# Optimization experiments

Measured on AMD Instinct MI355X. Metric: run time of the kernel, lower is better.

## Reference

```python
import jax, jax.numpy as jnp
import numpy as np

COMMITMENT_COST = 0.25


def setup_inputs() -> dict:
    key = jax.random.key(0)
    k1, k2 = jax.random.split(key)
    B, D, H, W, K = 32, 64, 64, 64, 1024
    z_e = jax.random.normal(k1, (B, D, H, W), dtype=jnp.float32)
    # codebook initialized uniform(-1/K, 1/K) as in the torch module
    embedding = jax.random.uniform(k2, (K, D), dtype=jnp.float32,
                                   minval=-1.0 / K, maxval=1.0 / K)
    return {"z_e": z_e, "embedding": embedding}


def reference(z_e, embedding):
    B, D, H, W = z_e.shape
    # [B,D,H,W] -> [N, D] with N = B*H*W
    z_flat = jnp.transpose(z_e, (0, 2, 3, 1)).reshape(-1, D)
    # squared L2 distances [N, K] via expansion (same math as torch)
    dists = (jnp.sum(z_flat * z_flat, axis=1, keepdims=True)
             + jnp.sum(embedding * embedding, axis=1)
             - 2.0 * jnp.matmul(z_flat, embedding.T))
    indices_flat = jnp.argmin(dists, axis=1)            # [N]
    z_q_flat = embedding[indices_flat]                  # gather [N, D]
    z_q = jnp.transpose(z_q_flat.reshape(B, H, W, D), (0, 3, 1, 2))
    # straight-through estimator
    z_q_st = z_e + jax.lax.stop_gradient(z_q - z_e)
    vq_loss = jnp.mean((z_q - jax.lax.stop_gradient(z_e)) ** 2)
    commitment_loss = COMMITMENT_COST * jnp.mean((z_e - jax.lax.stop_gradient(z_q)) ** 2)
    indices = indices_flat.reshape(B, H, W)
    return z_q_st, indices, vq_loss, commitment_loss
```

## Files before the change

### kernel.cpp

```cpp
#include <hip/hip_runtime.h>

#define BB 32
#define DD 64
#define HWSZ 4096
#define KK 1024
#define NPIX (BB*HWSZ)
#define NELEM (NPIX*DD)

#define IDX_OUT_OFF NELEM
#define LOSS_OFF (IDX_OUT_OFF + NPIX)

#define WS_E2    0
#define WS_EBH   4096
#define WS_EBL   (WS_EBH + KK*DD*2)
#define WS_IDX   (WS_EBL + KK*DD*2)
#define WS_LIST  (WS_IDX + NPIX*4)
#define WS_CNT   (WS_LIST + NPIX*4)
#define WS_PART  (WS_CNT + 64)
#define WS_ZROWS (WS_PART + 8192)

#define PXB 128
#define ZSTR 129

#define BAND 2e-4f

typedef __attribute__((ext_vector_type(8))) short short8v;
typedef __attribute__((ext_vector_type(4))) float float4v;

__device__ __forceinline__ unsigned short bf16_rne(float f) {
    unsigned u = __float_as_uint(f);
    u += 0x7fffu + ((u >> 16) & 1u);
    return (unsigned short)(u >> 16);
}
__device__ __forceinline__ float bf16_tof(unsigned short h) {
    return __uint_as_float(((unsigned)h) << 16);
}

__device__ __forceinline__ float np_sumsq64(const float* a) {
#pragma clang fp contract(off)
    float r0=0.f,r1=0.f,r2=0.f,r3=0.f,r4=0.f,r5=0.f,r6=0.f,r7=0.f;
#pragma unroll
    for (int i = 0; i < 64; i += 8) {
        r0 += a[i+0]*a[i+0]; r1 += a[i+1]*a[i+1];
        r2 += a[i+2]*a[i+2]; r3 += a[i+3]*a[i+3];
        r4 += a[i+4]*a[i+4]; r5 += a[i+5]*a[i+5];
        r6 += a[i+6]*a[i+6]; r7 += a[i+7]*a[i+7];
    }
    return ((r0+r1)+(r2+r3))+((r4+r5)+(r6+r7));
}

__device__ __forceinline__ float np_sumsq64_lds(const float* sh) {
#pragma clang fp contract(off)
    float r0=0.f,r1=0.f,r2=0.f,r3=0.f,r4=0.f,r5=0.f,r6=0.f,r7=0.f;
#pragma unroll
    for (int i = 0; i < 64; i += 8) {
        float a0=sh[i+0],a1=sh[i+1],a2=sh[i+2],a3=sh[i+3];
        float a4=sh[i+4],a5=sh[i+5],a6=sh[i+6],a7=sh[i+7];
        r0 += a0*a0; r1 += a1*a1; r2 += a2*a2; r3 += a3*a3;
        r4 += a4*a4; r5 += a5*a5; r6 += a6*a6; r7 += a7*a7;
    }
    return ((r0+r1)+(r2+r3))+((r4+r5)+(r6+r7));
}

__device__ __forceinline__ float np_sumsq64_str(const float* sh, int stride) {
#pragma clang fp contract(off)
    float r0=0.f,r1=0.f,r2=0.f,r3=0.f,r4=0.f,r5=0.f,r6=0.f,r7=0.f;
#pragma unroll
    for (int i = 0; i < 64; i += 8) {
        float a0=sh[(i+0)*stride],a1=sh[(i+1)*stride];
        float a2=sh[(i+2)*stride],a3=sh[(i+3)*stride];
        float a4=sh[(i+4)*stride],a5=sh[(i+5)*stride];
        float a6=sh[(i+6)*stride],a7=sh[(i+7)*stride];
        r0 += a0*a0; r1 += a1*a1; r2 += a2*a2; r3 += a3*a3;
        r4 += a4*a4; r5 += a5*a5; r6 += a6*a6; r7 += a7*a7;
    }
    return ((r0+r1)+(r2+r3))+((r4+r5)+(r6+r7));
}

__global__ __launch_bounds__(256) void vq_e2(const float* __restrict__ emb,
                                             float* __restrict__ e2) {
    int k = blockIdx.x * blockDim.x + threadIdx.x;
    float ek[DD];
    const float4* p = reinterpret_cast<const float4*>(emb + (size_t)k * DD);
#pragma unroll
    for (int q = 0; q < 16; ++q) {
        float4 v = p[q];
        ek[4*q+0]=v.x; ek[4*q+1]=v.y; ek[4*q+2]=v.z; ek[4*q+3]=v.w;
    }
    e2[k] = np_sumsq64(ek);
}

__global__ __launch_bounds__(256) void vq_bfrag(const float* __restrict__ emb,
                                                short* __restrict__ ebh,
                                                short* __restrict__ ebl) {
    int t    = blockIdx.x * 256 + threadIdx.x;
    int l    = t & 63;
    int slot = t >> 6;
    int ct = slot >> 1, ks = slot & 1;
    int code  = ct*16 + (l & 15);
    int dbase = ks*32 + (l >> 4)*8;
    const float* ep = emb + (size_t)code*DD + dbase;
    short8v h, lo;
#pragma unroll
    for (int j = 0; j < 8; ++j) {
        float v = ep[j];
        unsigned short hh = bf16_rne(v);
        h[j]  = (short)hh;
        lo[j] = (short)bf16_rne(v - bf16_tof(hh));
    }
    ((short8v*)ebh)[t] = h;
    ((short8v*)ebl)[t] = lo;
}

__global__ __launch_bounds__(256) void vq_main(
        const float* __restrict__ z, const float* __restrict__ emb,
        const short* __restrict__ ebh, const short* __restrict__ ebl,
        const float* __restrict__ e2,
        int* __restrict__ idx, int* __restrict__ list, int* __restrict__ cnt,
        float* __restrict__ zrows, int zcap,
        float* __restrict__ out, double* __restrict__ partial) {
    __shared__ float zsh[DD * ZSTR];
    __shared__ int   idx_loc[PXB];
    __shared__ int   flpx[128], flslot[128];
    __shared__ int   q_px[128], q_k1[128], q_k2[128];
    __shared__ int   nfl, n2c;
    __shared__ double sred[256];
    const int tid = threadIdx.x;
    const int w   = tid >> 6;
    const int l   = tid & 63;
    const int lr  = l & 15;
    const int lg  = l >> 4;
    const int b   = blockIdx.x >> 5;
    const int hw0 = (blockIdx.x & 31) * PXB;
    const float* zb = z + (size_t)b*(DD*HWSZ) + hw0;

    if (tid == 0) { nfl = 0; n2c = 0; }
    {
        const int row = tid >> 7, col = tid & 127;
#pragma unroll 8
        for (int d0 = 0; d0 < DD; d0 += 2)
            zsh[(d0+row)*ZSTR + col] = zb[(size_t)(d0+row)*HWSZ + col];
    }
    __syncthreads();

    short8v ah[2][2], al[2][2];
#pragma unroll
    for (int rt = 0; rt < 2; ++rt) {
#pragma unroll
        for (int ks = 0; ks < 2; ++ks) {
            int px = w*32 + rt*16 + lr;
            int dbase = ks*32 + lg*8;
#pragma unroll
            for (int j = 0; j < 8; ++j) {
                float v = zsh[(dbase + j)*ZSTR + px];
                unsigned short hh = bf16_rne(v);
                ah[rt][ks][j] = (short)hh;
                al[rt][ks][j] = (short)bf16_rne(v - bf16_tof(hh));
            }
        }
    }

    float b1a[2][4], b2a[2][4], b3a[2][4];
#pragma unroll
    for (int rt = 0; rt < 2; ++rt)
#pragma unroll
        for (int r = 0; r < 4; ++r) {
            b1a[rt][r] = 3.4e38f; b2a[rt][r] = 3.4e38f; b3a[rt][r] = 3.4e38f;
        }

    const short8v* EBH = (const short8v*)ebh;
    const short8v* EBL = (const short8v*)ebl;

    short8v bh0 = EBH[l],  bh1 = EBH[64 + l];
    short8v bl0 = EBL[l],  bl1 = EBL[64 + l];
    float   e2c = e2[lr];

#pragma unroll 1
    for (int ct = 0; ct < 64; ++ct) {
        int ctn = (ct + 1) & 63;
        int s0  = ctn*128 + l;
        short8v nh0 = EBH[s0], nh1 = EBH[s0+64];
        short8v nl0 = EBL[s0], nl1 = EBL[s0+64];
        float   ne2 = e2[ctn*16 + lr];

        const unsigned kf = (unsigned)(ct*16 + lr);
        const unsigned kr = kf ^ 1023u;
#pragma unroll
        for (int rt = 0; rt < 2; ++rt) {
            float4v acc = {0.f, 0.f, 0.f, 0.f};
            acc = __builtin_amdgcn_mfma_f32_16x16x32_bf16(ah[rt][0], bh0, acc, 0,0,0);
            acc = __builtin_amdgcn_mfma_f32_16x16x32_bf16(ah[rt][1], bh1, acc, 0,0,0);
            acc = __builtin_amdgcn_mfma_f32_16x16x32_bf16(ah[rt][0], bl0, acc, 0,0,0);
            acc = __builtin_amdgcn_mfma_f32_16x16x32_bf16(ah[rt][1], bl1, acc, 0,0,0);
            acc = __builtin_amdgcn_mfma_f32_16x16x32_bf16(al[rt][0], bh0, acc, 0,0,0);
            acc = __builtin_amdgcn_mfma_f32_16x16x32_bf16(al[rt][1], bh1, acc, 0,0,0);
#pragma unroll
            for (int r = 0; r < 4; ++r) {
                float s = __builtin_fmaf(-2.f, acc[r], e2c);
                unsigned su = __float_as_uint(s) & ~1023u;
                unsigned kk = ((int)su < 0) ? kr : kf;
                float p = __uint_as_float(su | kk);
                float ob2 = b2a[rt][r];
                b3a[rt][r] = fminf(b3a[rt][r], fmaxf(ob2, p));
                b2a[rt][r] = fmaxf(b1a[rt][r], fminf(ob2, p));
                b1a[rt][r] = fminf(b1a[rt][r], p);
            }
        }
        bh0 = nh0; bh1 = nh1; bl0 = nl0; bl1 = nl1; e2c = ne2;
    }

#pragma unroll
    for (int rt = 0; rt < 2; ++rt) {
#pragma unroll
        for (int r = 0; r < 4; ++r) {
            float b1 = b1a[rt][r], b2 = b2a[rt][r], b3 = b3a[rt][r];
#pragma unroll
            for (int m = 1; m < 16; m <<= 1) {
                float o1 = __shfl_xor(b1, m, 64);
                float o2 = __shfl_xor(b2, m, 64);
                float o3 = __shfl_xor(b3, m, 64);
                float mx  = fmaxf(b1, o1);
                float mn2 = fminf(b2, o2);
                float n1 = fminf(b1, o1);
                float n2 = fminf(mx, mn2);
                float n3 = fminf(fminf(fmaxf(mn2, mx), fmaxf(b2, o2)),
                                 fminf(b3, o3));
                b1 = n1; b2 = n2; b3 = n3;
            }
            if (lr == 0) {
                unsigned u1 = __float_as_uint(b1);
                int i1 = (int)(u1 & 1023u); if ((int)u1 < 0) i1 ^= 1023;
                int pxl = w*32 + rt*16 + lg*4 + r;
                int n   = b*HWSZ + hw0 + pxl;
                idx[n] = i1;
                idx_loc[pxl] = i1;
                if (b2 - b1 <= BAND) {
                    if (b3 - b1 <= BAND) {
                        int p = atomicAdd(cnt, 1);
                        list[p] = n;
                        int j = atomicAdd(&nfl, 1);
                        flpx[j] = pxl; flslot[j] = p;
                    } else {
                        unsigned u2 = __float_as_uint(b2);
                        int i2 = (int)(u2 & 1023u); if ((int)u2 < 0) i2 ^= 1023;
                        int j = atomicAdd(&n2c, 1);
                        q_px[j] = pxl; q_k1[j] = i1; q_k2[j] = i2;
                    }
                }
            }
        }
    }

    __syncthreads();
    if (tid < n2c) {
        int px = q_px[tid], k1 = q_k1[tid], k2 = q_k2[tid];
        float z2 = np_sumsq64_str(&zsh[px], ZSTR);
        const float* ep1 = emb + (size_t)k1 * DD;
        const float* ep2 = emb + (size_t)k2 * DD;
        float s1 = 0.f, s2 = 0.f;
#pragma unroll
        for (int d = 0; d < DD; ++d) {
            float zd = zsh[d*ZSTR + px];
            s1 = __builtin_fmaf(zd, ep1[d], s1);
            s2 = __builtin_fmaf(zd, ep2[d], s2);
        }
        float B1v, B2v;
        {
#pragma clang fp contract(off)
            float A1 = z2 + e2[k1]; B1v = __builtin_fmaf(-2.f, s1, A1);
            float A2 = z2 + e2[k2]; B2v = __builtin_fmaf(-2.f, s2, A2);
        }
        int win;
        if (k1 < k2) win = (B2v < B1v) ? k2 : k1;
        else         win = (B1v < B2v) ? k1 : k2;
        idx[b*HWSZ + hw0 + px] = win;
        idx_loc[px] = win;
    }

    __syncthreads();
    int nf = nfl;
    for (int j0 = 0; j0 < nf; j0 += 4) {
        int jj = j0 + (tid >> 6);
        if (jj < nf) {
            int slot = flslot[jj];
            if (slot < zcap) {
                int d = tid & 63;
                zrows[(size_t)slot*64 + d] = zsh[d*ZSTR + flpx[jj]];
            }
        }
    }
    __syncthreads();

    {
        const int px = tid & 127;
        const int dh = tid >> 7;
        const int ki = idx_loc[px];
        const float4* ep = reinterpret_cast<const float4*>(
                               emb + (size_t)ki*DD + dh*32);
        float* op = out + (size_t)b*(DD*HWSZ) + (size_t)(dh*32)*HWSZ + hw0 + px;
        float lsum = 0.f;
#pragma unroll
        for (int q = 0; q < 8; ++q) {
            float4 v = ep[q];
            int d = dh*32 + 4*q;
            float z0 = zsh[(d+0)*ZSTR + px];
            float z1 = zsh[(d+1)*ZSTR + px];
            float z2v = zsh[(d+2)*ZSTR + px];
            float z3 = zsh[(d+3)*ZSTR + px];
            op[(size_t)(4*q+0)*HWSZ] = v.x;
            op[(size_t)(4*q+1)*HWSZ] = v.y;
            op[(size_t)(4*q+2)*HWSZ] = v.z;
            op[(size_t)(4*q+3)*HWSZ] = v.w;
            float f0 = v.x - z0, f1 = v.y - z1, f2 = v.z - z2v, f3 = v.w - z3;
            lsum = __builtin_fmaf(f0, f0, lsum);
            lsum = __builtin_fmaf(f1, f1, lsum);
            lsum = __builtin_fmaf(f2, f2, lsum);
            lsum = __builtin_fmaf(f3, f3, lsum);
        }
        if (dh == 0) out[IDX_OUT_OFF + b*HWSZ + hw0 + px] = (float)ki;
        sred[tid] = (double)lsum;
    }
    __syncthreads();
#pragma unroll
    for (int sdown = 128; sdown > 0; sdown >>= 1) {
        if (tid < sdown) sred[tid] += sred[tid + sdown];
        __syncthreads();
    }
    if (tid == 0) partial[blockIdx.x] = sred[0];
}

__global__ __launch_bounds__(256) void vq_exact8(
        const float* __restrict__ z, const float* __restrict__ emb,
        const float* __restrict__ e2, const float* __restrict__ zrows,
        const int* __restrict__ list, const int* __restrict__ cnt,
        int zcap, int* __restrict__ idx, float* __restrict__ out,
        double* __restrict__ delta) {
    __shared__ float zsh[DD];
    __shared__ float rbv[256];
    __shared__ int   rbi[256];
    __shared__ double dred[64];
    const int tid = threadIdx.x;
    const int C   = *cnt;

    for (int i = blockIdx.x; i < C; i += gridDim.x) {
        const int n = list[i];
        if (tid < 64) {
            if (i < zcap) {
                zsh[tid] = zrows[(size_t)i*64 + tid];
            } else {
                zsh[tid] = z[(size_t)(n>>12)*(DD*HWSZ) + (n&4095)
                             + (size_t)tid*HWSZ];
            }
        }
        __syncthreads();

        const float z2 = np_sumsq64_lds(zsh);

        float bestv = 3.4e38f; int bi = 0x7fffffff;
#pragma unroll
        for (int c = 0; c < 4; ++c) {
            int k = c*256 + tid;
            const float4* ep = reinterpret_cast<const float4*>(emb + (size_t)k*DD);
            float s = 0.f;
#pragma unroll
            for (int q = 0; q < 16; ++q) {
                float4 v = ep[q];
                s = __builtin_fmaf(zsh[4*q+0], v.x, s);
                s = __builtin_fmaf(zsh[4*q+1], v.y, s);
                s = __builtin_fmaf(zsh[4*q+2], v.z, s);
                s = __builtin_fmaf(zsh[4*q+3], v.w, s);
            }
            float Bv;
            {
#pragma clang fp contract(off)
                float A = z2 + e2[k];
                Bv = __builtin_fmaf(-2.f, s, A);
            }
            if (Bv < bestv) { bestv = Bv; bi = k; }
        }

        rbv[tid] = bestv; rbi[tid] = bi;
        __syncthreads();
#pragma unroll
        for (int sdown = 128; sdown > 0; sdown >>= 1) {
            if (tid < sdown) {
                float ov = rbv[tid + sdown]; int oi = rbi[tid + sdown];
                if (ov < rbv[tid] || (ov == rbv[tid] && oi < rbi[tid])) {
                    rbv[tid] = ov; rbi[tid] = oi;
                }
            }
            __syncthreads();
        }
        const int win = rbi[0];
        const int old = idx[n];
        if (win != old) {
            const int bq = n >> 12, hw = n & 4095;
            if (tid < 64) {
                float zd = zsh[tid];
                float en = emb[(size_t)win*DD + tid];
                float eo = emb[(size_t)old*DD + tid];
                out[(size_t)bq*(DD*HWSZ) + (size_t)tid*HWSZ + hw] = en;
                float dn = en - zd, dl = eo - zd;
                dred[tid] = (double)(dn*dn) - (double)(dl*dl);
            }
            __syncthreads();
            if (tid == 0) {
                double s = 0.0;
                for (int j = 0; j < 64; ++j) s += dred[j];
                atomicAdd(delta, s);
                idx[n] = win;
                out[IDX_OUT_OFF + n] = (float)win;
            }
        }
        __syncthreads();
    }
}

__global__ __launch_bounds__(256) void vq_finalize(
        const double* __restrict__ part, const double* __restrict__ delta,
        float* __restrict__ out) {
    __shared__ double sred[256];
    int t = threadIdx.x;
    sred[t] = part[t] + part[t + 256] + part[t + 512] + part[t + 768];
    __syncthreads();
#pragma unroll
    for (int sdown = 128; sdown > 0; sdown >>= 1) {
        if (t < sdown) sred[t] += sred[t + sdown];
        __syncthreads();
    }
    if (t == 0) {
        double m = (sred[0] + *delta) / (double)NELEM;
        out[LOSS_OFF]     = (float)m;
        out[LOSS_OFF + 1] = (float)(0.25 * m);
    }
}

extern "C" void kernel_launch(void* const* d_in, const int* in_sizes, int n_in,
                              void* d_out, int out_size, void* d_ws, size_t ws_size,
                              hipStream_t stream) {
    const float* z   = (const float*)d_in[0];
    const float* emb = (const float*)d_in[1];
    float* out = (float*)d_out;
    char*  ws  = (char*)d_ws;

    float*  e2p   = (float*)(ws + WS_E2);
    short*  ebh   = (short*)(ws + WS_EBH);
    short*  ebl   = (short*)(ws + WS_EBL);
    int*    idxp  = (int*)(ws + WS_IDX);
    int*    lst   = (int*)(ws + WS_LIST);
    int*    cntp  = (int*)(ws + WS_CNT);
    double* delta = (double*)(ws + WS_CNT + 8);
    double* part  = (double*)(ws + WS_PART);
    float*  zrows = (float*)(ws + WS_ZROWS);

    long long zrem = (long long)ws_size - (long long)WS_ZROWS;
    int zcap = zrem > 0 ? (int)(zrem / 256) : 0;
    if (zcap > NPIX) zcap = NPIX;

    hipMemsetAsync(cntp, 0, 16, stream);
    vq_e2       <<<KK/256,   256, 0, stream>>>(emb, e2p);
    vq_bfrag    <<<32,       256, 0, stream>>>(emb, ebh, ebl);
    vq_main     <<<NPIX/PXB, 256, 0, stream>>>(z, emb, ebh, ebl, e2p, idxp,
                                               lst, cntp, zrows, zcap,
                                               out, part);
    vq_exact8   <<<512,      256, 0, stream>>>(z, emb, e2p, zrows, lst, cntp,
                                               zcap, idxp, out, delta);
    vq_finalize <<<1,        256, 0, stream>>>(part, delta, out);
}
```

Measured before the change: 133.2 us.

## Shift distance scores positive to simplify top-3 tracking; fuse prep kernels

Result: slower. 136.5 us (+2.5%).

```diff
diff --git a/kernel.cpp b/kernel.cpp
--- a/kernel.cpp
+++ b/kernel.cpp
@@ -22,7 +22,8 @@
 #define PXB 128
 #define ZSTR 129
 
-#define BAND 2e-4f
+#define SHIFT 0.25f
+#define BAND 2.5e-4f
 
 typedef __attribute__((ext_vector_type(8))) short short8v;
 typedef __attribute__((ext_vector_type(4))) float float4v;
@@ -77,22 +78,10 @@
     return ((r0+r1)+(r2+r3))+((r4+r5)+(r6+r7));
 }
 
-__global__ __launch_bounds__(256) void vq_e2(const float* __restrict__ emb,
-                                             float* __restrict__ e2) {
-    int k = blockIdx.x * blockDim.x + threadIdx.x;
-    float ek[DD];
-    const float4* p = reinterpret_cast<const float4*>(emb + (size_t)k * DD);
-#pragma unroll
-    for (int q = 0; q < 16; ++q) {
-        float4 v = p[q];
-        ek[4*q+0]=v.x; ek[4*q+1]=v.y; ek[4*q+2]=v.z; ek[4*q+3]=v.w;
-    }
-    e2[k] = np_sumsq64(ek);
-}
-
-__global__ __launch_bounds__(256) void vq_bfrag(const float* __restrict__ emb,
-                                                short* __restrict__ ebh,
-                                                short* __restrict__ ebl) {
+__global__ __launch_bounds__(256) void vq_prep(const float* __restrict__ emb,
+                                               short* __restrict__ ebh,
+                                               short* __restrict__ ebl,
+                                               float* __restrict__ e2) {
     int t    = blockIdx.x * 256 + threadIdx.x;
     int l    = t & 63;
     int slot = t >> 6;
@@ -110,6 +99,18 @@
     }
     ((short8v*)ebh)[t] = h;
     ((short8v*)ebl)[t] = lo;
+
+    if (blockIdx.x < 4) {
+        int k = blockIdx.x * 256 + threadIdx.x;
+        float ek[DD];
+        const float4* p = reinterpret_cast<const float4*>(emb + (size_t)k * DD);
+#pragma unroll
+        for (int q = 0; q < 16; ++q) {
+            float4 v = p[q];
+            ek[4*q+0]=v.x; ek[4*q+1]=v.y; ek[4*q+2]=v.z; ek[4*q+3]=v.w;
+        }
+        e2[k] = np_sumsq64(ek);
+    }
 }
 
 __global__ __launch_bounds__(256) void vq_main(
@@ -173,18 +174,17 @@
 
     short8v bh0 = EBH[l],  bh1 = EBH[64 + l];
     short8v bl0 = EBL[l],  bl1 = EBL[64 + l];
-    float   e2c = e2[lr];
-
-#pragma unroll 1
+    float   e2c = e2[lr] + SHIFT;
+
+#pragma unroll 2
     for (int ct = 0; ct < 64; ++ct) {
         int ctn = (ct + 1) & 63;
         int s0  = ctn*128 + l;
         short8v nh0 = EBH[s0], nh1 = EBH[s0+64];
         short8v nl0 = EBL[s0], nl1 = EBL[s0+64];
-        float   ne2 = e2[ctn*16 + lr];
+        float   ne2 = e2[ctn*16 + lr] + SHIFT;
 
         const unsigned kf = (unsigned)(ct*16 + lr);
-        const unsigned kr = kf ^ 1023u;
 #pragma unroll
         for (int rt = 0; rt < 2; ++rt) {
             float4v acc = {0.f, 0.f, 0.f, 0.f};
@@ -197,13 +197,12 @@
 #pragma unroll
             for (int r = 0; r < 4; ++r) {
                 float s = __builtin_fmaf(-2.f, acc[r], e2c);
-                unsigned su = __float_as_uint(s) & ~1023u;
-                unsigned kk = ((int)su < 0) ? kr : kf;
-                float p = __uint_as_float(su | kk);
-                float ob2 = b2a[rt][r];
-                b3a[rt][r] = fminf(b3a[rt][r], fmaxf(ob2, p));
-                b2a[rt][r] = fmaxf(b1a[rt][r], fminf(ob2, p));
-                b1a[rt][r] = fminf(b1a[rt][r], p);
+                float p = __uint_as_float(
+                    (__float_as_uint(s) & ~1023u) | kf);
+                float ob1 = b1a[rt][r], ob2 = b2a[rt][r];
+                b1a[rt][r] = fminf(ob1, p);
+                b2a[rt][r] = __builtin_amdgcn_fmed3f(ob1, ob2, p);
+                b3a[rt][r] = __builtin_amdgcn_fmed3f(ob2, b3a[rt][r], p);
             }
         }
         bh0 = nh0; bh1 = nh1; bl0 = nl0; bl1 = nl1; e2c = ne2;
@@ -228,8 +227,7 @@
                 b1 = n1; b2 = n2; b3 = n3;
             }
             if (lr == 0) {
-                unsigned u1 = __float_as_uint(b1);
-                int i1 = (int)(u1 & 1023u); if ((int)u1 < 0) i1 ^= 1023;
+                int i1 = (int)(__float_as_uint(b1) & 1023u);
                 int pxl = w*32 + rt*16 + lg*4 + r;
                 int n   = b*HWSZ + hw0 + pxl;
                 idx[n] = i1;
@@ -241,8 +239,7 @@
                         int j = atomicAdd(&nfl, 1);
                         flpx[j] = pxl; flslot[j] = p;
                     } else {
-                        unsigned u2 = __float_as_uint(b2);
-                        int i2 = (int)(u2 & 1023u); if ((int)u2 < 0) i2 ^= 1023;
+                        int i2 = (int)(__float_as_uint(b2) & 1023u);
                         int j = atomicAdd(&n2c, 1);
                         q_px[j] = pxl; q_k1[j] = i1; q_k2[j] = i2;
                     }
@@ -458,8 +455,7 @@
     if (zcap > NPIX) zcap = NPIX;
 
     hipMemsetAsync(cntp, 0, 16, stream);
-    vq_e2       <<<KK/256,   256, 0, stream>>>(emb, e2p);
-    vq_bfrag    <<<32,       256, 0, stream>>>(emb, ebh, ebl);
+    vq_prep     <<<32,       256, 0, stream>>>(emb, ebh, ebl, e2p);
     vq_main     <<<NPIX/PXB, 256, 0, stream>>>(z, emb, ebh, ebl, e2p, idxp,
                                                lst, cntp, zrows, zcap,
                                                out, part);
```
